# Kernel tuning notes

Hardware: AMD Instinct MI355X
Metric: run time of the kernel (lower is better)

Reference implementation:

```python
import jax, jax.numpy as jnp
import numpy as np

N_HEADS = 4
D_K = 64
SCALE = D_K ** (-0.5)


def setup_inputs() -> dict:
    key = jax.random.key(0)
    k1, k2, k3, k4, k5 = jax.random.split(key, 5)
    B, C, H, W = 32, 256, 32, 32
    x = jax.random.normal(k1, (B, C, H, W), dtype=jnp.float32)
    proj_w = jax.random.normal(k2, (N_HEADS * D_K * 3, C), dtype=jnp.float32) * 0.02
    proj_b = jax.random.normal(k3, (N_HEADS * D_K * 3,), dtype=jnp.float32) * 0.02
    out_w = jax.random.normal(k4, (C, N_HEADS * D_K), dtype=jnp.float32) * 0.02
    out_b = jax.random.normal(k5, (C,), dtype=jnp.float32) * 0.02
    return {"x": x, "proj_w": proj_w, "proj_b": proj_b, "out_w": out_w, "out_b": out_b}


def reference(x, proj_w, proj_b, out_w, out_b):
    B, C, H, W = x.shape
    # [B, C, H, W] -> [B, N, C] with N = H*W
    xs = x.reshape(B, C, H * W).transpose(0, 2, 1)
    # fused QKV projection (torch Linear: y = x @ W.T + b)
    qkv = (xs @ proj_w.T + proj_b).reshape(B, H * W, N_HEADS, 3 * D_K)
    q, k, v = jnp.split(qkv, 3, axis=-1)  # each [B, N, h, d_k]
    # full score tensor [B, i, j, h] (the original materializes this)
    scores = jnp.einsum('bihd,bjhd->bijh', q, k) * SCALE
    attn = jax.nn.softmax(scores, axis=2)  # softmax over keys j
    ctx = jnp.einsum('bijh,bjhd->bihd', attn, v).reshape(B, H * W, N_HEADS * D_K)
    out = ctx @ out_w.T + out_b + xs  # output proj + residual (note: GroupNorm unused in orig forward)
    return out.transpose(0, 2, 1).reshape(B, C, H, W)
```

## Files before the change

kernel.cpp:

```cpp
#include <hip/hip_runtime.h>
#include <hip/hip_bf16.h>

#define BB  32
#define CC  256
#define NN  1024
#define NHH 4
#define DKK 64
#define QD  768
#define QSCALE 0.18033688011112042f

typedef __bf16 bf16;
typedef __bf16 bf16x8 __attribute__((ext_vector_type(8)));
typedef float  f32x4  __attribute__((ext_vector_type(4)));
typedef float  f32x16 __attribute__((ext_vector_type(16)));

typedef __attribute__((address_space(1))) const void g_void;
typedef __attribute__((address_space(3))) void l_void;

__global__ __launch_bounds__(256) void k_prep_w(const float* __restrict__ proj_w,
                                                const float* __restrict__ out_w,
                                                bf16* __restrict__ pwt,
                                                bf16* __restrict__ owt) {
    int i = blockIdx.x * 256 + threadIdx.x;
    if (i < QD * CC) {
        int o = i / CC;
        float v = proj_w[i];
        if ((o % 192) < DKK) v *= QSCALE;
        pwt[i] = (bf16)v;
    }
    if (i < CC * CC) {
        owt[i] = (bf16)out_w[i];
    }
}

__global__ __launch_bounds__(256) void k_transpose_x(const float* __restrict__ x,
                                                     bf16* __restrict__ xs) {
    int bid = blockIdx.x;
    int nt = bid & 15;
    int ct = (bid >> 4) & 3;
    int b  = bid >> 6;
    __shared__ float lds[64][65];
    int t = threadIdx.x;
    const float* xp = x + ((size_t)b * CC + ct * 64) * NN + nt * 64;
#pragma unroll
    for (int rep = 0; rep < 16; ++rep) {
        int idx = rep * 256 + t;
        int c = idx >> 6, n = idx & 63;
        lds[c][n] = xp[(size_t)c * NN + n];
    }
    __syncthreads();
    bf16* xo = xs + ((size_t)b * NN + nt * 64) * CC + ct * 64;
#pragma unroll
    for (int rep = 0; rep < 16; ++rep) {
        int idx = rep * 256 + t;
        int c = idx & 63, n = idx >> 6;
        xo[(size_t)n * CC + c] = (bf16)lds[c][n];
    }
}

__global__ __launch_bounds__(256, 4) void k_gemm_qkv(const bf16* __restrict__ A,
                                                     const bf16* __restrict__ Bw,
                                                     const float* __restrict__ bias,
                                                     bf16* __restrict__ qkv,
                                                     bf16* __restrict__ vt) {
    int l = (blockIdx.x & 7) * 192 + (blockIdx.x >> 3);
    int mtile = l / 6, ntile = l % 6;
    int wave = threadIdx.x >> 6, lane = threadIdx.x & 63;
    int wm = wave >> 1, wn = wave & 1;
    int lr = lane & 15, lg = lane >> 4;
    int row0 = mtile * 128, col0 = ntile * 128;

    __shared__ __align__(16) bf16 Abuf[2][4096];
    __shared__ __align__(16) bf16 Bbuf[2][4096];

    int srow = lane >> 2, sc = lane & 3;
    int rA0 = wave * 16 + srow, rA1 = (wave + 4) * 16 + srow;
    const bf16* a0 = A + (size_t)(row0 + rA0) * CC + ((sc ^ ((rA0 >> 1) & 3)) * 8);
    const bf16* a1 = A + (size_t)(row0 + rA1) * CC + ((sc ^ ((rA1 >> 1) & 3)) * 8);
    const bf16* b0 = Bw + (size_t)(col0 + rA0) * CC + ((sc ^ ((rA0 >> 1) & 3)) * 8);
    const bf16* b1 = Bw + (size_t)(col0 + rA1) * CC + ((sc ^ ((rA1 >> 1) & 3)) * 8);

#define STAGE(ks, sel)                                                          \
    do {                                                                        \
        __builtin_amdgcn_global_load_lds((g_void*)(a0 + (ks) * 32),             \
            (l_void*)&Abuf[sel][wave * 512], 16, 0, 0);                         \
        __builtin_amdgcn_global_load_lds((g_void*)(a1 + (ks) * 32),             \
            (l_void*)&Abuf[sel][(wave + 4) * 512], 16, 0, 0);                   \
        __builtin_amdgcn_global_load_lds((g_void*)(b0 + (ks) * 32),             \
            (l_void*)&Bbuf[sel][wave * 512], 16, 0, 0);                         \
        __builtin_amdgcn_global_load_lds((g_void*)(b1 + (ks) * 32),             \
            (l_void*)&Bbuf[sel][(wave + 4) * 512], 16, 0, 0);                   \
    } while (0)

    f32x4 acc[4][4] = {};
    STAGE(0, 0);
    asm volatile("s_waitcnt vmcnt(0)" ::: "memory");
    __builtin_amdgcn_s_barrier();

    int cur = 0;
    for (int ks = 0; ks < 8; ++ks) {
        if (ks + 1 < 8) STAGE(ks + 1, cur ^ 1);
        bf16x8 af[4], bfm[4];
#pragma unroll
        for (int mt = 0; mt < 4; ++mt) {
            int row = wm * 64 + mt * 16 + lr;
            af[mt] = *reinterpret_cast<const bf16x8*>(
                &Abuf[cur][row * 32 + ((lg ^ ((row >> 1) & 3)) * 8)]);
        }
#pragma unroll
        for (int nt = 0; nt < 4; ++nt) {
            int row = wn * 64 + nt * 16 + lr;
            bfm[nt] = *reinterpret_cast<const bf16x8*>(
                &Bbuf[cur][row * 32 + ((lg ^ ((row >> 1) & 3)) * 8)]);
        }
#pragma unroll
        for (int mt = 0; mt < 4; ++mt)
#pragma unroll
            for (int nt = 0; nt < 4; ++nt)
                acc[mt][nt] = __builtin_amdgcn_mfma_f32_16x16x32_bf16(
                    af[mt], bfm[nt], acc[mt][nt], 0, 0, 0);
        asm volatile("s_waitcnt vmcnt(0)" ::: "memory");
        __builtin_amdgcn_s_barrier();
        cur ^= 1;
    }
#undef STAGE

#pragma unroll
    for (int nt = 0; nt < 4; ++nt) {
        int col = col0 + wn * 64 + nt * 16 + lr;
        int sect = col % 192;
        int h = col / 192;
        float bv = bias[col];
        if (sect < DKK) bv *= QSCALE;
#pragma unroll
        for (int mt = 0; mt < 4; ++mt) {
            int rowb = row0 + wm * 64 + mt * 16 + lg * 4;
            if (sect < 128) {
#pragma unroll
                for (int rr = 0; rr < 4; ++rr)
                    qkv[(size_t)(rowb + rr) * QD + col] =
                        (bf16)(acc[mt][nt][rr] + bv);
            } else {
                int d = sect - 128;
                int b = rowb >> 10, n = rowb & 1023;
                int kb = n >> 5, j = n & 31;
                unsigned u0, u1;
                asm("v_cvt_pk_bf16_f32 %0, %1, %2" : "=v"(u0)
                    : "v"(acc[mt][nt][0] + bv), "v"(acc[mt][nt][1] + bv));
                asm("v_cvt_pk_bf16_f32 %0, %1, %2" : "=v"(u1)
                    : "v"(acc[mt][nt][2] + bv), "v"(acc[mt][nt][3] + bv));
                *reinterpret_cast<uint2*>(
                    &vt[(((size_t)(b * NHH + h) * 32 + kb) * 64 + d) * 32 + j]) =
                    make_uint2(u0, u1);
            }
        }
    }
}

__global__ __launch_bounds__(256, 4) void k_attn(const bf16* __restrict__ qkv,
                                                 const bf16* __restrict__ vt,
                                                 bf16* __restrict__ ctx) {
    int bid = blockIdx.x;
    int qt = bid >> 7;
    int bh = bid & 127;
    int b  = bh >> 2;
    int h  = bh & 3;
    int wave = threadIdx.x >> 6, lane = threadIdx.x & 63;
    int lq = lane & 31, hi = lane >> 5;
    int q0 = qt * 128 + wave * 32;

    __shared__ __align__(16) bf16 Kbuf[2][2048];
    __shared__ __align__(16) bf16 Vbuf[2][2048];
    __shared__ bf16 tl[4][32][68];

    const bf16* qkb = qkv + (size_t)b * NN * QD;
    const bf16* qrow = qkb + (size_t)(q0 + lq) * QD + h * 192 + 8 * hi;
    bf16x8 qf[4];
#pragma unroll
    for (int dk = 0; dk < 4; ++dk)
        qf[dk] = *reinterpret_cast<const bf16x8*>(qrow + 16 * dk);

    const bf16* kglob = qkb + h * 192 + 64;
    const bf16* vtile = vt + (size_t)bh * 32 * 2048;

    int krow = wave * 8 + (lane >> 3), kc = lane & 7;
    const bf16* ksrc0 = kglob + (size_t)krow * QD + ((kc ^ (krow & 7)) * 8);
    int vrow = wave * 16 + (lane >> 2), vc = lane & 3;
    const bf16* vsrc0 = vtile + (size_t)vrow * 32 + ((vc ^ ((vrow >> 1) & 3)) * 8);

#define STAGE(kb, sel)                                                          \
    do {                                                                        \
        __builtin_amdgcn_global_load_lds(                                       \
            (g_void*)(ksrc0 + (size_t)(kb) * 32 * QD),                          \
            (l_void*)&Kbuf[sel][wave * 512], 16, 0, 0);                         \
        __builtin_amdgcn_global_load_lds(                                       \
            (g_void*)(vsrc0 + (size_t)(kb) * 2048),                             \
            (l_void*)&Vbuf[sel][wave * 512], 16, 0, 0);                         \
    } while (0)

    f32x16 acc0 = {}, acc1 = {};
    float m = -1e30f, l = 0.f;

    STAGE(0, 0);
    asm volatile("s_waitcnt vmcnt(0)" ::: "memory");
    __builtin_amdgcn_s_barrier();

    int cur = 0;
    for (int t = 0; t < 32; ++t) {
        if (t + 1 < 32) STAGE(t + 1, cur ^ 1);

        f32x16 s = {};
#pragma unroll
        for (int dk = 0; dk < 4; ++dk) {
            bf16x8 kf = *reinterpret_cast<const bf16x8*>(
                &Kbuf[cur][lq * 64 + (((dk * 2 + hi) ^ (lq & 7)) * 8)]);
            s = __builtin_amdgcn_mfma_f32_32x32x16_bf16(kf, qf[dk], s, 0, 0, 0);
        }
        bf16x8 vf[4];
        int sw = (lq >> 1) & 3;
        vf[0] = *reinterpret_cast<const bf16x8*>(
            &Vbuf[cur][lq * 32 + ((hi ^ sw) * 8)]);
        vf[1] = *reinterpret_cast<const bf16x8*>(
            &Vbuf[cur][lq * 32 + (((2 + hi) ^ sw) * 8)]);
        vf[2] = *reinterpret_cast<const bf16x8*>(
            &Vbuf[cur][(32 + lq) * 32 + ((hi ^ sw) * 8)]);
        vf[3] = *reinterpret_cast<const bf16x8*>(
            &Vbuf[cur][(32 + lq) * 32 + (((2 + hi) ^ sw) * 8)]);

        float t0, t1, t2t, t3;
        t0 = fmaxf(s[0], s[1]);  t1 = fmaxf(s[2], s[3]);
        t2t = fmaxf(s[4], s[5]); t3 = fmaxf(s[6], s[7]);
        t0 = fmaxf(t0, t1);      t2t = fmaxf(t2t, t3);
        float pm0 = fmaxf(t0, t2t);
        t0 = fmaxf(s[8], s[9]);   t1 = fmaxf(s[10], s[11]);
        t2t = fmaxf(s[12], s[13]); t3 = fmaxf(s[14], s[15]);
        t0 = fmaxf(t0, t1);       t2t = fmaxf(t2t, t3);
        float pm = fmaxf(pm0, fmaxf(t0, t2t));
        {
            float a = pm, b2 = pm;
            asm("v_permlane32_swap_b32 %0, %1" : "+v"(a), "+v"(b2));
            pm = fmaxf(a, b2);
        }
        if (__any(pm > m + 8.f)) {
            float nm = fmaxf(m, pm);
            float corr = __builtin_amdgcn_exp2f(m - nm);
            l *= corr;
            acc0 *= corr;
            acc1 *= corr;
            m = nm;
        }
        float ls = 0.f;
#pragma unroll
        for (int i = 0; i < 16; ++i) {
            s[i] = __builtin_amdgcn_exp2f(s[i] - m);
            ls += s[i];
        }
        l += ls;
        unsigned w[8];
#pragma unroll
        for (int g = 0; g < 2; ++g) {
#pragma unroll
            for (int j = 0; j < 4; ++j) {
                unsigned tw;
                asm("v_cvt_pk_bf16_f32 %0, %1, %2"
                    : "=v"(tw) : "v"(s[8 * g + 2 * j]), "v"(s[8 * g + 2 * j + 1]));
                w[4 * g + j] = tw;
            }
            asm("v_permlane32_swap_b32 %0, %1" : "+v"(w[4 * g + 0]), "+v"(w[4 * g + 2]));
            asm("v_permlane32_swap_b32 %0, %1" : "+v"(w[4 * g + 1]), "+v"(w[4 * g + 3]));
        }
        union { unsigned u[4]; bf16x8 v; } pu0, pu1;
#pragma unroll
        for (int j = 0; j < 4; ++j) { pu0.u[j] = w[j]; pu1.u[j] = w[4 + j]; }

        acc0 = __builtin_amdgcn_mfma_f32_32x32x16_bf16(vf[0], pu0.v, acc0, 0, 0, 0);
        acc0 = __builtin_amdgcn_mfma_f32_32x32x16_bf16(vf[1], pu1.v, acc0, 0, 0, 0);
        acc1 = __builtin_amdgcn_mfma_f32_32x32x16_bf16(vf[2], pu0.v, acc1, 0, 0, 0);
        acc1 = __builtin_amdgcn_mfma_f32_32x32x16_bf16(vf[3], pu1.v, acc1, 0, 0, 0);

        asm volatile("s_waitcnt vmcnt(0)" ::: "memory");
        __builtin_amdgcn_s_barrier();
        cur ^= 1;
    }
#undef STAGE

    {
        float a = l, b2 = l;
        asm("v_permlane32_swap_b32 %0, %1" : "+v"(a), "+v"(b2));
        l = a + b2;
    }
    float inv = 1.0f / l;

#pragma unroll
    for (int r = 0; r < 16; ++r) {
        int d = (r & 3) + 8 * (r >> 2) + 4 * hi;
        tl[wave][lq][d]      = (bf16)(acc0[r] * inv);
        tl[wave][lq][d + 32] = (bf16)(acc1[r] * inv);
    }
    __syncthreads();
    bf16* cb = ctx + ((size_t)(b * NN + q0)) * 256 + h * 64;
#pragma unroll
    for (int r = 0; r < 4; ++r) {
        int q = 8 * r + (lane >> 3);
        int d0 = (lane & 7) * 8;
        uint2 lo  = *reinterpret_cast<const uint2*>(&tl[wave][q][d0]);
        uint2 hi2 = *reinterpret_cast<const uint2*>(&tl[wave][q][d0 + 4]);
        uint4 o4 = make_uint4(lo.x, lo.y, hi2.x, hi2.y);
        *reinterpret_cast<uint4*>(cb + (size_t)q * 256 + d0) = o4;
    }
}

__global__ __launch_bounds__(256, 4) void k_gemm_out(const bf16* __restrict__ A,
                                                     const bf16* __restrict__ Bw,
                                                     const float* __restrict__ bias,
                                                     const float* __restrict__ x,
                                                     float* __restrict__ out) {
    int l = (blockIdx.x & 7) * 128 + (blockIdx.x >> 3);
    int mtile = l >> 2, ntile = l & 3;
    int wave = threadIdx.x >> 6, lane = threadIdx.x & 63;
    int wm = wave >> 1, wn = wave & 1;
    int lr = lane & 15, lg = lane >> 4;
    int row0 = mtile * 128, col0 = ntile * 64;

    __shared__ __align__(16) bf16 Abuf[2][4096];
    __shared__ __align__(16) bf16 Bbuf[2][2048];

    int srow = lane >> 2, sc = lane & 3;
    int rA0 = wave * 16 + srow, rA1 = (wave + 4) * 16 + srow;
    const bf16* a0 = A + (size_t)(row0 + rA0) * CC + ((sc ^ ((rA0 >> 1) & 3)) * 8);
    const bf16* a1 = A + (size_t)(row0 + rA1) * CC + ((sc ^ ((rA1 >> 1) & 3)) * 8);
    const bf16* b0 = Bw + (size_t)(col0 + rA0) * CC + ((sc ^ ((rA0 >> 1) & 3)) * 8);

#define STAGE(ks, sel)                                                          \
    do {                                                                        \
        __builtin_amdgcn_global_load_lds((g_void*)(a0 + (ks) * 32),             \
            (l_void*)&Abuf[sel][wave * 512], 16, 0, 0);                         \
        __builtin_amdgcn_global_load_lds((g_void*)(a1 + (ks) * 32),             \
            (l_void*)&Abuf[sel][(wave + 4) * 512], 16, 0, 0);                   \
        __builtin_amdgcn_global_load_lds((g_void*)(b0 + (ks) * 32),             \
            (l_void*)&Bbuf[sel][wave * 512], 16, 0, 0);                         \
    } while (0)

    f32x4 acc[4][2] = {};
    STAGE(0, 0);
    asm volatile("s_waitcnt vmcnt(0)" ::: "memory");
    __builtin_amdgcn_s_barrier();

    int cur = 0;
    for (int ks = 0; ks < 8; ++ks) {
        if (ks + 1 < 8) STAGE(ks + 1, cur ^ 1);
        bf16x8 af[4], bfm[2];
#pragma unroll
        for (int mt = 0; mt < 4; ++mt) {
            int row = wm * 64 + mt * 16 + lr;
            af[mt] = *reinterpret_cast<const bf16x8*>(
                &Abuf[cur][row * 32 + ((lg ^ ((row >> 1) & 3)) * 8)]);
        }
#pragma unroll
        for (int nt = 0; nt < 2; ++nt) {
            int row = wn * 32 + nt * 16 + lr;
            bfm[nt] = *reinterpret_cast<const bf16x8*>(
                &Bbuf[cur][row * 32 + ((lg ^ ((row >> 1) & 3)) * 8)]);
        }
#pragma unroll
        for (int mt = 0; mt < 4; ++mt)
#pragma unroll
            for (int nt = 0; nt < 2; ++nt)
                acc[mt][nt] = __builtin_amdgcn_mfma_f32_16x16x32_bf16(
                    af[mt], bfm[nt], acc[mt][nt], 0, 0, 0);
        asm volatile("s_waitcnt vmcnt(0)" ::: "memory");
        __builtin_amdgcn_s_barrier();
        cur ^= 1;
    }
#undef STAGE

#pragma unroll
    for (int nt = 0; nt < 2; ++nt) {
        int c = col0 + wn * 32 + nt * 16 + lr;
        float bv = bias[c];
#pragma unroll
        for (int mt = 0; mt < 4; ++mt) {
            int rowb = row0 + wm * 64 + mt * 16 + lg * 4;
            int b = rowb >> 10, n = rowb & 1023;
            size_t o = ((size_t)b * CC + c) * NN + n;
            f32x4 xr = *reinterpret_cast<const f32x4*>(&x[o]);
            f32x4 r = acc[mt][nt] + bv + xr;
            *reinterpret_cast<f32x4*>(&out[o]) = r;
        }
    }
}

extern "C" void kernel_launch(void* const* d_in, const int* in_sizes, int n_in,
                              void* d_out, int out_size, void* d_ws, size_t ws_size,
                              hipStream_t stream) {
    const float* x      = (const float*)d_in[0];
    const float* proj_w = (const float*)d_in[1];
    const float* proj_b = (const float*)d_in[2];
    const float* out_w  = (const float*)d_in[3];
    const float* out_b  = (const float*)d_in[4];
    float* out = (float*)d_out;

    bf16* xs  = (bf16*)d_ws;
    bf16* qkv = xs + (size_t)32768 * 256;
    bf16* vt  = qkv + (size_t)32768 * 768;
    bf16* pwt = vt + (size_t)8388608;
    bf16* owt = pwt + (size_t)768 * 256;
    bf16* ctx = xs;

    k_prep_w     <<<dim3(768),  dim3(256), 0, stream>>>(proj_w, out_w, pwt, owt);
    k_transpose_x<<<dim3(2048), dim3(256), 0, stream>>>(x, xs);
    k_gemm_qkv   <<<dim3(1536), dim3(256), 0, stream>>>(xs, pwt, proj_b, qkv, vt);
    k_attn       <<<dim3(1024), dim3(256), 0, stream>>>(qkv, vt, ctx);
    k_gemm_out   <<<dim3(1024), dim3(256), 0, stream>>>(ctx, owt, out_b, x, out);
}
```

Baseline: 108.5 us.

## Double key-tile size to 64 in attention and unroll ping-pong buffers

The attention kernel now processes 64 keys per iteration (16 iterations instead of 32), with the transposed-V layout written by the QKV GEMM changed to 64-wide key blocks to match. The loop is manually unrolled into two fixed buffers, and all shared memory is merged into one array that is reused for the output transpose. Swizzles are recomputed for the wider tiles. The aim is to halve the barrier and wait overhead per key and give the scheduler more independent MFMA work, at the cost of more registers and a larger LDS footprint that may reduce occupancy.

```diff
diff --git a/kernel.cpp b/kernel.cpp
--- a/kernel.cpp
+++ b/kernel.cpp
@@ -143,14 +143,14 @@
             } else {
                 int d = sect - 128;
                 int b = rowb >> 10, n = rowb & 1023;
-                int kb = n >> 5, j = n & 31;
+                int kb = n >> 6, j = n & 63;
                 unsigned u0, u1;
                 asm("v_cvt_pk_bf16_f32 %0, %1, %2" : "=v"(u0)
                     : "v"(acc[mt][nt][0] + bv), "v"(acc[mt][nt][1] + bv));
                 asm("v_cvt_pk_bf16_f32 %0, %1, %2" : "=v"(u1)
                     : "v"(acc[mt][nt][2] + bv), "v"(acc[mt][nt][3] + bv));
                 *reinterpret_cast<uint2*>(
-                    &vt[(((size_t)(b * NHH + h) * 32 + kb) * 64 + d) * 32 + j]) =
+                    &vt[(((size_t)(b * NHH + h) * 16 + kb) * 64 + d) * 64 + j]) =
                     make_uint2(u0, u1);
             }
         }
@@ -169,9 +169,7 @@
     int lq = lane & 31, hi = lane >> 5;
     int q0 = qt * 128 + wave * 32;
 
-    __shared__ __align__(16) bf16 Kbuf[2][2048];
-    __shared__ __align__(16) bf16 Vbuf[2][2048];
-    __shared__ bf16 tl[4][32][68];
+    __shared__ __align__(16) bf16 smem[16384];
 
     const bf16* qkb = qkv + (size_t)b * NN * QD;
     const bf16* qrow = qkb + (size_t)(q0 + lq) * QD + h * 192 + 8 * hi;
@@ -181,108 +179,152 @@
         qf[dk] = *reinterpret_cast<const bf16x8*>(qrow + 16 * dk);
 
     const bf16* kglob = qkb + h * 192 + 64;
-    const bf16* vtile = vt + (size_t)bh * 32 * 2048;
-
-    int krow = wave * 8 + (lane >> 3), kc = lane & 7;
-    const bf16* ksrc0 = kglob + (size_t)krow * QD + ((kc ^ (krow & 7)) * 8);
-    int vrow = wave * 16 + (lane >> 2), vc = lane & 3;
-    const bf16* vsrc0 = vtile + (size_t)vrow * 32 + ((vc ^ ((vrow >> 1) & 3)) * 8);
-
-#define STAGE(kb, sel)                                                          \
-    do {                                                                        \
-        __builtin_amdgcn_global_load_lds(                                       \
-            (g_void*)(ksrc0 + (size_t)(kb) * 32 * QD),                          \
-            (l_void*)&Kbuf[sel][wave * 512], 16, 0, 0);                         \
-        __builtin_amdgcn_global_load_lds(                                       \
-            (g_void*)(vsrc0 + (size_t)(kb) * 2048),                             \
-            (l_void*)&Vbuf[sel][wave * 512], 16, 0, 0);                         \
-    } while (0)
+    const bf16* vtile = vt + (size_t)bh * 16 * 4096;
+
+    int srw = lane >> 3, sch = lane & 7;
+    int r0 = wave * 16 + srw;
+    int g0 = sch ^ srw ^ ((2 * wave) & 3);
+    int g1 = sch ^ srw ^ ((2 * wave + 1) & 3);
+    const bf16* kA0 = kglob + (size_t)r0 * QD + g0 * 8;
+    const bf16* kA1 = kglob + (size_t)(r0 + 8) * QD + g1 * 8;
+    const bf16* vA0 = vtile + r0 * 64 + g0 * 8;
+    const bf16* vA1 = vtile + (r0 + 8) * 64 + g1 * 8;
+
+    int swzl = (lq & 7) ^ (lq >> 3);
+    int adK[4];
+#pragma unroll
+    for (int i = 0; i < 4; ++i)
+        adK[i] = lq * 64 + (((2 * i) | hi) ^ swzl) * 8;
 
     f32x16 acc0 = {}, acc1 = {};
     float m = -1e30f, l = 0.f;
+
+#define STAGE(t, BUF)                                                           \
+    do {                                                                        \
+        size_t ko = (size_t)(t) * 64 * QD;                                      \
+        size_t vo = (size_t)(t) * 4096;                                         \
+        __builtin_amdgcn_global_load_lds((g_void*)(kA0 + ko),                   \
+            (l_void*)&smem[(BUF) * 4096 + wave * 1024], 16, 0, 0);              \
+        __builtin_amdgcn_global_load_lds((g_void*)(kA1 + ko),                   \
+            (l_void*)&smem[(BUF) * 4096 + wave * 1024 + 512], 16, 0, 0);        \
+        __builtin_amdgcn_global_load_lds((g_void*)(vA0 + vo),                   \
+            (l_void*)&smem[8192 + (BUF) * 4096 + wave * 1024], 16, 0, 0);       \
+        __builtin_amdgcn_global_load_lds((g_void*)(vA1 + vo),                   \
+            (l_void*)&smem[8192 + (BUF) * 4096 + wave * 1024 + 512], 16, 0, 0); \
+    } while (0)
+
+#define MAX3(a, b, c) fmaxf(fmaxf((a), (b)), (c))
+
+#define COMPUTE(BUF)                                                            \
+    do {                                                                        \
+        f32x16 s0 = {}, s1 = {};                                                \
+        _Pragma("unroll")                                                       \
+        for (int dk = 0; dk < 4; ++dk) {                                        \
+            bf16x8 kf0 = *reinterpret_cast<const bf16x8*>(                      \
+                &smem[adK[dk] + (BUF) * 4096]);                                 \
+            bf16x8 kf1 = *reinterpret_cast<const bf16x8*>(                      \
+                &smem[adK[dk] + (BUF) * 4096 + 2048]);                          \
+            s0 = __builtin_amdgcn_mfma_f32_32x32x16_bf16(kf0, qf[dk], s0, 0, 0, 0); \
+            s1 = __builtin_amdgcn_mfma_f32_32x32x16_bf16(kf1, qf[dk], s1, 0, 0, 0); \
+        }                                                                       \
+        float x0 = MAX3(s0[0], s0[1], s0[2]);                                   \
+        float x1 = MAX3(s0[3], s0[4], s0[5]);                                   \
+        float x2 = MAX3(s0[6], s0[7], s0[8]);                                   \
+        float x3 = MAX3(s0[9], s0[10], s0[11]);                                 \
+        float x4 = MAX3(s0[12], s0[13], s0[14]);                                \
+        float x5 = MAX3(s1[0], s1[1], s1[2]);                                   \
+        float x6 = MAX3(s1[3], s1[4], s1[5]);                                   \
+        float x7 = MAX3(s1[6], s1[7], s1[8]);                                   \
+        float x8 = MAX3(s1[9], s1[10], s1[11]);                                 \
+        float x9 = MAX3(s1[12], s1[13], s1[14]);                                \
+        float xa = fmaxf(s0[15], s1[15]);                                       \
+        x0 = MAX3(x0, x1, x2);                                                  \
+        x3 = MAX3(x3, x4, x5);                                                  \
+        x6 = MAX3(x6, x7, x8);                                                  \
+        x9 = MAX3(x9, xa, x0);                                                  \
+        x3 = fmaxf(x3, x6);                                                     \
+        float pm = fmaxf(x9, x3);                                               \
+        {                                                                       \
+            float a_ = pm, b_ = pm;                                             \
+            asm("v_permlane32_swap_b32 %0, %1" : "+v"(a_), "+v"(b_));           \
+            pm = fmaxf(a_, b_);                                                 \
+        }                                                                       \
+        if (__any(pm > m + 8.f)) {                                              \
+            float nm = fmaxf(m, pm);                                            \
+            float corr = __builtin_amdgcn_exp2f(m - nm);                        \
+            l *= corr; acc0 *= corr; acc1 *= corr; m = nm;                      \
+        }                                                                       \
+        _Pragma("unroll")                                                       \
+        for (int i = 0; i < 16; ++i) {                                          \
+            s0[i] = __builtin_amdgcn_exp2f(s0[i] - m);                          \
+            s1[i] = __builtin_amdgcn_exp2f(s1[i] - m);                          \
+        }                                                                       \
+        {                                                                       \
+            float l0 = (s0[0] + s0[1]) + (s0[2] + s0[3]);                       \
+            float l1 = (s0[4] + s0[5]) + (s0[6] + s0[7]);                       \
+            float l2 = (s0[8] + s0[9]) + (s0[10] + s0[11]);                     \
+            float l3 = (s0[12] + s0[13]) + (s0[14] + s0[15]);                   \
+            float l4 = (s1[0] + s1[1]) + (s1[2] + s1[3]);                       \
+            float l5 = (s1[4] + s1[5]) + (s1[6] + s1[7]);                       \
+            float l6 = (s1[8] + s1[9]) + (s1[10] + s1[11]);                     \
+            float l7 = (s1[12] + s1[13]) + (s1[14] + s1[15]);                   \
+            l += ((l0 + l1) + (l2 + l3)) + ((l4 + l5) + (l6 + l7));             \
+        }                                                                       \
+        union { unsigned u[4]; bf16x8 v; } pu[4];                               \
+        _Pragma("unroll")                                                       \
+        for (int g = 0; g < 2; ++g) {                                           \
+            unsigned w0, w1, w2, w3;                                            \
+            asm("v_cvt_pk_bf16_f32 %0, %1, %2" : "=v"(w0)                       \
+                : "v"(s0[8 * g + 0]), "v"(s0[8 * g + 1]));                      \
+            asm("v_cvt_pk_bf16_f32 %0, %1, %2" : "=v"(w1)                       \
+                : "v"(s0[8 * g + 2]), "v"(s0[8 * g + 3]));                      \
+            asm("v_cvt_pk_bf16_f32 %0, %1, %2" : "=v"(w2)                       \
+                : "v"(s0[8 * g + 4]), "v"(s0[8 * g + 5]));                      \
+            asm("v_cvt_pk_bf16_f32 %0, %1, %2" : "=v"(w3)                       \
+                : "v"(s0[8 * g + 6]), "v"(s0[8 * g + 7]));                      \
+            asm("v_permlane32_swap_b32 %0, %1" : "+v"(w0), "+v"(w2));           \
+            asm("v_permlane32_swap_b32 %0, %1" : "+v"(w1), "+v"(w3));           \
+            pu[g].u[0] = w0; pu[g].u[1] = w1; pu[g].u[2] = w2; pu[g].u[3] = w3; \
+            asm("v_cvt_pk_bf16_f32 %0, %1, %2" : "=v"(w0)                       \
+                : "v"(s1[8 * g + 0]), "v"(s1[8 * g + 1]));                      \
+            asm("v_cvt_pk_bf16_f32 %0, %1, %2" : "=v"(w1)                       \
+                : "v"(s1[8 * g + 2]), "v"(s1[8 * g + 3]));                      \
+            asm("v_cvt_pk_bf16_f32 %0, %1, %2" : "=v"(w2)                       \
+                : "v"(s1[8 * g + 4]), "v"(s1[8 * g + 5]));                      \
+            asm("v_cvt_pk_bf16_f32 %0, %1, %2" : "=v"(w3)                       \
+                : "v"(s1[8 * g + 6]), "v"(s1[8 * g + 7]));                      \
+            asm("v_permlane32_swap_b32 %0, %1" : "+v"(w0), "+v"(w2));           \
+            asm("v_permlane32_swap_b32 %0, %1" : "+v"(w1), "+v"(w3));           \
+            pu[2 + g].u[0] = w0; pu[2 + g].u[1] = w1;                           \
+            pu[2 + g].u[2] = w2; pu[2 + g].u[3] = w3;                           \
+        }                                                                       \
+        _Pragma("unroll")                                                       \
+        for (int kk = 0; kk < 4; ++kk) {                                        \
+            bf16x8 v0_ = *reinterpret_cast<const bf16x8*>(                      \
+                &smem[adK[kk] + 8192 + (BUF) * 4096]);                          \
+            bf16x8 v1_ = *reinterpret_cast<const bf16x8*>(                      \
+                &smem[adK[kk] + 8192 + (BUF) * 4096 + 2048]);                   \
+            acc0 = __builtin_amdgcn_mfma_f32_32x32x16_bf16(v0_, pu[kk].v, acc0, 0, 0, 0); \
+            acc1 = __builtin_amdgcn_mfma_f32_32x32x16_bf16(v1_, pu[kk].v, acc1, 0, 0, 0); \
+        }                                                                       \
+    } while (0)
 
     STAGE(0, 0);
     asm volatile("s_waitcnt vmcnt(0)" ::: "memory");
     __builtin_amdgcn_s_barrier();
 
-    int cur = 0;
-    for (int t = 0; t < 32; ++t) {
-        if (t + 1 < 32) STAGE(t + 1, cur ^ 1);
-
-        f32x16 s = {};
-#pragma unroll
-        for (int dk = 0; dk < 4; ++dk) {
-            bf16x8 kf = *reinterpret_cast<const bf16x8*>(
-                &Kbuf[cur][lq * 64 + (((dk * 2 + hi) ^ (lq & 7)) * 8)]);
-            s = __builtin_amdgcn_mfma_f32_32x32x16_bf16(kf, qf[dk], s, 0, 0, 0);
-        }
-        bf16x8 vf[4];
-        int sw = (lq >> 1) & 3;
-        vf[0] = *reinterpret_cast<const bf16x8*>(
-            &Vbuf[cur][lq * 32 + ((hi ^ sw) * 8)]);
-        vf[1] = *reinterpret_cast<const bf16x8*>(
-            &Vbuf[cur][lq * 32 + (((2 + hi) ^ sw) * 8)]);
-        vf[2] = *reinterpret_cast<const bf16x8*>(
-            &Vbuf[cur][(32 + lq) * 32 + ((hi ^ sw) * 8)]);
-        vf[3] = *reinterpret_cast<const bf16x8*>(
-            &Vbuf[cur][(32 + lq) * 32 + (((2 + hi) ^ sw) * 8)]);
-
-        float t0, t1, t2t, t3;
-        t0 = fmaxf(s[0], s[1]);  t1 = fmaxf(s[2], s[3]);
-        t2t = fmaxf(s[4], s[5]); t3 = fmaxf(s[6], s[7]);
-        t0 = fmaxf(t0, t1);      t2t = fmaxf(t2t, t3);
-        float pm0 = fmaxf(t0, t2t);
-        t0 = fmaxf(s[8], s[9]);   t1 = fmaxf(s[10], s[11]);
-        t2t = fmaxf(s[12], s[13]); t3 = fmaxf(s[14], s[15]);
-        t0 = fmaxf(t0, t1);       t2t = fmaxf(t2t, t3);
-        float pm = fmaxf(pm0, fmaxf(t0, t2t));
-        {
-            float a = pm, b2 = pm;
-            asm("v_permlane32_swap_b32 %0, %1" : "+v"(a), "+v"(b2));
-            pm = fmaxf(a, b2);
-        }
-        if (__any(pm > m + 8.f)) {
-            float nm = fmaxf(m, pm);
-            float corr = __builtin_amdgcn_exp2f(m - nm);
-            l *= corr;
-            acc0 *= corr;
-            acc1 *= corr;
-            m = nm;
-        }
-        float ls = 0.f;
-#pragma unroll
-        for (int i = 0; i < 16; ++i) {
-            s[i] = __builtin_amdgcn_exp2f(s[i] - m);
-            ls += s[i];
-        }
-        l += ls;
-        unsigned w[8];
-#pragma unroll
-        for (int g = 0; g < 2; ++g) {
-#pragma unroll
-            for (int j = 0; j < 4; ++j) {
-                unsigned tw;
-                asm("v_cvt_pk_bf16_f32 %0, %1, %2"
-                    : "=v"(tw) : "v"(s[8 * g + 2 * j]), "v"(s[8 * g + 2 * j + 1]));
-                w[4 * g + j] = tw;
-            }
-            asm("v_permlane32_swap_b32 %0, %1" : "+v"(w[4 * g + 0]), "+v"(w[4 * g + 2]));
-            asm("v_permlane32_swap_b32 %0, %1" : "+v"(w[4 * g + 1]), "+v"(w[4 * g + 3]));
-        }
-        union { unsigned u[4]; bf16x8 v; } pu0, pu1;
-#pragma unroll
-        for (int j = 0; j < 4; ++j) { pu0.u[j] = w[j]; pu1.u[j] = w[4 + j]; }
-
-        acc0 = __builtin_amdgcn_mfma_f32_32x32x16_bf16(vf[0], pu0.v, acc0, 0, 0, 0);
-        acc0 = __builtin_amdgcn_mfma_f32_32x32x16_bf16(vf[1], pu1.v, acc0, 0, 0, 0);
-        acc1 = __builtin_amdgcn_mfma_f32_32x32x16_bf16(vf[2], pu0.v, acc1, 0, 0, 0);
-        acc1 = __builtin_amdgcn_mfma_f32_32x32x16_bf16(vf[3], pu1.v, acc1, 0, 0, 0);
-
+    for (int t = 0; t < 16; t += 2) {
+        STAGE(t + 1, 1);
+        COMPUTE(0);
         asm volatile("s_waitcnt vmcnt(0)" ::: "memory");
         __builtin_amdgcn_s_barrier();
-        cur ^= 1;
+        if (t + 2 < 16) STAGE(t + 2, 0);
+        COMPUTE(1);
+        asm volatile("s_waitcnt vmcnt(0)" ::: "memory");
+        __builtin_amdgcn_s_barrier();
     }
 #undef STAGE
+#undef COMPUTE
 
     {
         float a = l, b2 = l;
@@ -291,11 +333,12 @@
     }
     float inv = 1.0f / l;
 
+    bf16* tl = &smem[(size_t)wave * 32 * 68];
 #pragma unroll
     for (int r = 0; r < 16; ++r) {
         int d = (r & 3) + 8 * (r >> 2) + 4 * hi;
-        tl[wave][lq][d]      = (bf16)(acc0[r] * inv);
-        tl[wave][lq][d + 32] = (bf16)(acc1[r] * inv);
+        tl[lq * 68 + d]      = (bf16)(acc0[r] * inv);
+        tl[lq * 68 + d + 32] = (bf16)(acc1[r] * inv);
     }
     __syncthreads();
     bf16* cb = ctx + ((size_t)(b * NN + q0)) * 256 + h * 64;
@@ -303,8 +346,8 @@
     for (int r = 0; r < 4; ++r) {
         int q = 8 * r + (lane >> 3);
         int d0 = (lane & 7) * 8;
-        uint2 lo  = *reinterpret_cast<const uint2*>(&tl[wave][q][d0]);
-        uint2 hi2 = *reinterpret_cast<const uint2*>(&tl[wave][q][d0 + 4]);
+        uint2 lo  = *reinterpret_cast<const uint2*>(&tl[q * 68 + d0]);
+        uint2 hi2 = *reinterpret_cast<const uint2*>(&tl[q * 68 + d0 + 4]);
         uint4 o4 = make_uint4(lo.x, lo.y, hi2.x, hi2.y);
         *reinterpret_cast<uint4*>(cb + (size_t)q * 256 + d0) = o4;
     }
```

Result: faster. 102.8 us (-5.3%).
